# Kernel optimization log

Hardware: AMD Instinct MI355X
Metric: run time of the kernel (lower is better)

## Reference

```python
import jax, jax.numpy as jnp
import numpy as np

D_MODEL = 256
D_STATE = 1
HEADDIM = 32
NHEADS = D_MODEL // HEADDIM
HH = 64
WW = 64
BATCH = 2
L = HH * WW
D_IN_PROJ = (2 * D_MODEL + 2 * D_STATE + NHEADS) * 4


def _part1by1(n):
    n = n.astype(np.int64) & 0xFFFF
    n = (n | (n << 8)) & 0x00FF00FF
    n = (n | (n << 4)) & 0x0F0F0F0F
    n = (n | (n << 2)) & 0x33333333
    n = (n | (n << 1)) & 0x55555555
    return n


def _morton_indices(H, W):
    ys, xs = np.meshgrid(np.arange(H), np.arange(W), indexing='ij')
    ys, xs = ys.ravel(), xs.ravel()
    code_H = _part1by1(xs) | (_part1by1(ys) << 1)  # horizontal-first z-order
    code_V = _part1by1(ys) | (_part1by1(xs) << 1)  # vertical-first z-order
    mh = np.argsort(code_H, kind='stable').astype(np.int32)
    mv = np.argsort(code_V, kind='stable').astype(np.int32)
    ih = np.empty_like(mh); ih[mh] = np.arange(mh.size, dtype=np.int32)
    iv = np.empty_like(mv); iv[mv] = np.arange(mv.size, dtype=np.int32)
    return mh, mv, ih, iv


def setup_inputs() -> dict:
    key = jax.random.key(0)
    ks = jax.random.split(key, 12)
    x = jax.random.normal(ks[0], (BATCH, D_MODEL, HH, WW), dtype=jnp.float32)
    # RoPE tables: angles for L positions, HEADDIM/2 freqs
    freqs = 1.0 / (10000.0 ** (np.arange(0, HEADDIM, 2, dtype=np.float32) / HEADDIM))
    ang = np.outer(np.arange(L, dtype=np.float32), freqs)
    freqs_cos = jnp.asarray(np.cos(ang), dtype=jnp.float32)
    freqs_sin = jnp.asarray(np.sin(ang), dtype=jnp.float32)
    mh, mv, ih, iv = _morton_indices(HH, WW)
    # parameters
    W_in = jax.random.normal(ks[1], (D_MODEL, D_IN_PROJ), dtype=jnp.float32) * 0.02
    W_out = jax.random.normal(ks[2], (4 * D_MODEL, D_MODEL), dtype=jnp.float32) * 0.02
    conv_w = jax.random.normal(ks[3], (4, 2 * D_MODEL, 2 * D_MODEL, 3, 3), dtype=jnp.float32) * 0.02
    bn_gamma = jnp.ones((4, 2 * D_MODEL), dtype=jnp.float32)
    bn_beta = jnp.zeros((4, 2 * D_MODEL), dtype=jnp.float32)
    bn_mean = jax.random.normal(ks[4], (4, 2 * D_MODEL), dtype=jnp.float32) * 0.1
    bn_var = jax.random.uniform(ks[5], (4, 2 * D_MODEL), dtype=jnp.float32) * 0.5 + 0.5
    # dt bias init per module: inv softplus of dt ~ LogUniform(1e-3, 1e-1)
    u = np.asarray(jax.random.uniform(ks[6], (4, NHEADS)))
    dt = np.exp(u * (np.log(0.1) - np.log(0.001)) + np.log(0.001))
    dt_bias = jnp.asarray(dt + np.log(-np.expm1(-dt)), dtype=jnp.float32)
    A_log = jnp.log(jax.random.uniform(ks[7], (4, NHEADS), minval=1.0, maxval=16.0)).astype(jnp.float32)
    D = jnp.ones((4, NHEADS), dtype=jnp.float32)
    ln_gamma = jnp.ones((D_MODEL,), dtype=jnp.float32)
    ln_beta = jnp.zeros((D_MODEL,), dtype=jnp.float32)
    return dict(x=x, freqs_cos=freqs_cos, freqs_sin=freqs_sin,
                morton_H=jnp.asarray(mh), morton_V=jnp.asarray(mv),
                inv_H=jnp.asarray(ih), inv_V=jnp.asarray(iv),
                W_in=W_in, conv_w=conv_w, bn_gamma=bn_gamma, bn_beta=bn_beta,
                bn_mean=bn_mean, bn_var=bn_var, dt_bias=dt_bias, A_log=A_log,
                D=D, W_out=W_out, ln_gamma=ln_gamma, ln_beta=ln_beta)


def _rope(xh, cos, sin):
    # xh: [B,L,nh,hd]; complex multiply on (even,odd) pairs, matching view_as_complex
    xr, xi = xh[..., 0::2], xh[..., 1::2]
    c = cos[None, :, None, :]
    s = sin[None, :, None, :]
    out_r = xr * c - xi * s
    out_i = xr * s + xi * c
    return jnp.stack([out_r, out_i], axis=-1).reshape(xh.shape)


def _forward(x, freqs_cos, freqs_sin, morton_H, morton_V, inv_H, inv_V,
             W_in, conv_w, bn_gamma, bn_beta, bn_mean, bn_var,
             dt_bias, A_log, D, W_out, ln_gamma, ln_beta):
    B, C, H, W = x.shape
    Lh = H * W
    dim, ds, nh, hd = C, D_STATE, NHEADS, HEADDIM
    xf = x.reshape(B, C, Lh).transpose(0, 2, 1)            # [B,L,C]
    zxbcdt = xf @ W_in                                      # [B,L,d_in_proj]
    per = dim + (dim + 2 * ds) + nh
    specs = [(morton_H, inv_H, False), (morton_H, inv_H, True),
             (morton_V, inv_V, False), (morton_V, inv_V, True)]
    outs = []
    for d, (idx, iidx, flip) in enumerate(specs):
        blk = zxbcdt[..., d * per:(d + 1) * per]
        z = blk[..., :dim]
        xBC = blk[..., dim:2 * dim + 2 * ds]
        dt = blk[..., 2 * dim + 2 * ds:]
        xd, Bd, Cd = xBC[..., :dim], xBC[..., dim:dim + ds], xBC[..., dim + ds:]
        # depth-refine x,z with 3x3 conv + GELU + BN (eval)
        xz = jnp.concatenate([xd, z], axis=-1).transpose(0, 2, 1).reshape(B, 2 * C, H, W)
        xz = jax.lax.conv_general_dilated(xz, conv_w[d], (1, 1), 'SAME',
                                          dimension_numbers=('NCHW', 'OIHW', 'NCHW'))
        xz = jax.nn.gelu(xz)
        xz = (xz - bn_mean[d][None, :, None, None]) * jax.lax.rsqrt(bn_var[d] + 1e-3)[None, :, None, None] \
             * bn_gamma[d][None, :, None, None] + bn_beta[d][None, :, None, None]
        xz = xz.reshape(B, 2 * C, Lh).transpose(0, 2, 1)
        xd, zd = xz[..., :dim], xz[..., dim:]
        # morton reorder (+ flip for backward directions)
        def reord(a):
            a = jnp.take(a, idx, axis=1)
            return jnp.flip(a, axis=1) if flip else a
        xd, zd, Bd, Cd, dt = reord(xd), reord(zd), reord(Bd), reord(Cd), reord(dt)
        xh = _rope(xd.reshape(B, Lh, nh, hd), freqs_cos, freqs_sin)
        dtv = jax.nn.softplus(dt + dt_bias[d])              # [B,L,nh]
        A = -jnp.exp(A_log[d])                              # [nh]
        a = jnp.exp(dtv * A)                                # [B,L,nh]
        bterm = (dtv[..., None, None] * xh[..., None]) * Bd[:, :, None, None, :]  # [B,L,nh,hd,ds]
        def comb(c1, c2):
            a1, b1 = c1
            a2, b2 = c2
            return (a1 * a2, b1 * a2 + b2)
        _, h = jax.lax.associative_scan(comb, (a[..., None, None], bterm), axis=1)
        y = jnp.einsum('blhps,bls->blhp', h, Cd) + D[d][None, None, :, None] * xh
        y = y.reshape(B, Lh, dim) * (zd * jax.nn.sigmoid(zd))  # SiLU gate
        if flip:
            y = jnp.flip(y, axis=1)
        y = jnp.take(y, iidx, axis=1)                       # inverse morton
        outs.append(y)
    out = jnp.concatenate(outs, axis=-1) @ W_out            # [B,L,C]
    mu = out.mean(-1, keepdims=True)
    var = ((out - mu) ** 2).mean(-1, keepdims=True)
    out = (out - mu) * jax.lax.rsqrt(var + 1e-6) * ln_gamma + ln_beta
    return out.transpose(0, 2, 1).reshape(B, C, H, W)


def reference(x, freqs_cos, freqs_sin, morton_H, morton_V, inv_H, inv_V,
              W_in, conv_w, bn_gamma, bn_beta, bn_mean, bn_var,
              dt_bias, A_log, D, W_out, ln_gamma, ln_beta):
    return _forward(x, freqs_cos, freqs_sin, morton_H, morton_V, inv_H, inv_V,
                    W_in, conv_w, bn_gamma, bn_beta, bn_mean, bn_var,
                    dt_bias, A_log, D, W_out, ln_gamma, ln_beta)
```

## Files before the change

kernel.cpp:

```cpp
#include <hip/hip_runtime.h>
#include <math.h>

#define BATCH 2
#define CDIM 256
#define LLEN 4096
#define NH 8
#define HD 32
#define PER 522
#define NPROJ 2088
#define NPROJ_PAD 2112

typedef __attribute__((ext_vector_type(8))) short short8;
typedef __attribute__((ext_vector_type(4))) float f32x4;

static __device__ __forceinline__ ushort f2bf(float f) {
    unsigned u = __float_as_uint(f);
    u += 0x7fffu + ((u >> 16) & 1u);
    return (ushort)(u >> 16);
}
static __device__ __forceinline__ float bf2f(ushort u) {
    return __uint_as_float(((unsigned)u) << 16);
}

__global__ __launch_bounds__(256) void convert_wt(
    const float* __restrict__ W, ushort* __restrict__ Wt, int K, int N)
{
    __shared__ float tile[32][33];
    int n0 = blockIdx.x * 32, k0 = blockIdx.y * 32;
    int t = threadIdx.x;
    int nl = t & 31, kl = t >> 5;
    #pragma unroll
    for (int i = 0; i < 4; i++) {
        int n = n0 + nl;
        tile[kl + i * 8][nl] = (n < N) ? W[(long)(k0 + kl + i * 8) * N + n] : 0.f;
    }
    __syncthreads();
    int kl2 = t & 31, nl2 = t >> 5;
    #pragma unroll
    for (int i = 0; i < 4; i++)
        Wt[(long)(n0 + nl2 + i * 8) * K + k0 + kl2] = f2bf(tile[kl2][nl2 + i * 8]);
}

__global__ __launch_bounds__(256) void convert_x(
    const float* __restrict__ x, ushort* __restrict__ xbf)
{
    __shared__ float tile[32][33];
    int l0 = blockIdx.x * 32, c0 = blockIdx.y * 32, b = blockIdx.z;
    int t = threadIdx.x;
    int ll = t & 31, cl = t >> 5;
    #pragma unroll
    for (int i = 0; i < 4; i++)
        tile[cl + i * 8][ll] = x[((long)b * CDIM + c0 + cl + i * 8) * LLEN + l0 + ll];
    __syncthreads();
    int cl2 = t & 31, ll2 = t >> 5;
    #pragma unroll
    for (int i = 0; i < 4; i++)
        xbf[((long)b * LLEN + l0 + ll2 + i * 8) * CDIM + c0 + cl2] = f2bf(tile[cl2][ll2 + i * 8]);
}

__global__ __launch_bounds__(256) void convert_w(
    const float* __restrict__ cw, ushort* __restrict__ wbf)
{
    __shared__ ushort tmp[4608];
    int blk = blockIdx.x;
    int t = threadIdx.x;
    const float* src = cw + (long)blk * 4608;
    for (int q = t; q < 4608; q += 256) tmp[q] = f2bf(src[q]);
    __syncthreads();
    int d = blk >> 9, co = blk & 511;
    for (int q = t; q < 4608; q += 256) {
        int tt = q >> 9, ci = q & 511;
        wbf[(((long)(d * 9 + tt) * 512 + co) << 9) + ci] = tmp[ci * 9 + tt];
    }
}

__global__ __launch_bounds__(256) void gemm_in(
    const ushort* __restrict__ A, const ushort* __restrict__ Bt,
    ushort* __restrict__ cinb, float* __restrict__ bcdt)
{
    __shared__ ushort As[128][72];
    __shared__ ushort Bs[64][72];
    const int K = CDIM;
    int m0 = blockIdx.x * 128, n0 = blockIdx.y * 64;
    int t = threadIdx.x;
    int wave = t >> 6, lane = t & 63;
    int l15 = lane & 15, ko = lane >> 4;
    int mbase = wave * 32;

    f32x4 acc[2][4];
    #pragma unroll
    for (int mt = 0; mt < 2; mt++)
        #pragma unroll
        for (int nt = 0; nt < 4; nt++) acc[mt][nt] = (f32x4){0.f, 0.f, 0.f, 0.f};

    for (int k0 = 0; k0 < K; k0 += 64) {
        #pragma unroll
        for (int i = 0; i < 4; i++) {
            int g = t + 256 * i;
            int row = g >> 3, grp = g & 7;
            *(uint4*)&As[row][grp * 8] = *(const uint4*)&A[(long)(m0 + row) * K + k0 + grp * 8];
        }
        #pragma unroll
        for (int i = 0; i < 2; i++) {
            int g = t + 256 * i;
            int row = g >> 3, grp = g & 7;
            *(uint4*)&Bs[row][grp * 8] = *(const uint4*)&Bt[(long)(n0 + row) * K + k0 + grp * 8];
        }
        __syncthreads();
        #pragma unroll
        for (int kk = 0; kk < 2; kk++) {
            short8 a0 = *(const short8*)&As[mbase + l15][kk * 32 + ko * 8];
            short8 a1 = *(const short8*)&As[mbase + 16 + l15][kk * 32 + ko * 8];
            short8 bb[4];
            #pragma unroll
            for (int nt = 0; nt < 4; nt++)
                bb[nt] = *(const short8*)&Bs[nt * 16 + l15][kk * 32 + ko * 8];
            #pragma unroll
            for (int nt = 0; nt < 4; nt++) {
                acc[0][nt] = __builtin_amdgcn_mfma_f32_16x16x32_bf16(a0, bb[nt], acc[0][nt], 0, 0, 0);
                acc[1][nt] = __builtin_amdgcn_mfma_f32_16x16x32_bf16(a1, bb[nt], acc[1][nt], 0, 0, 0);
            }
        }
        __syncthreads();
    }
    #pragma unroll
    for (int nt = 0; nt < 4; nt++) {
        int n = n0 + nt * 16 + l15;
        if (n < NPROJ) {
            int d = n / PER;
            int r = n - d * PER;
            #pragma unroll
            for (int mt = 0; mt < 2; mt++)
                #pragma unroll
                for (int reg = 0; reg < 4; reg++) {
                    int m = m0 + mbase + mt * 16 + ko * 4 + reg;
                    int b = m >> 12, l = m & (LLEN - 1);
                    float v = acc[mt][nt][reg];
                    if (r < 512) {
                        int ch = (r < 256) ? (256 + r) : (r - 256);
                        cinb[(((long)d * BATCH + b) * LLEN + l) * 512 + ch] = f2bf(v);
                    } else {
                        bcdt[(long)m * 48 + d * 12 + (r - 512)] = v;
                    }
                }
        }
    }
}

__global__ __launch_bounds__(256) void gemm_bt(
    const ushort* __restrict__ A, const ushort* __restrict__ Bt, float* __restrict__ C,
    int K, int N)
{
    __shared__ ushort As[128][72];
    __shared__ ushort Bs[64][72];
    int m0 = blockIdx.x * 128, n0 = blockIdx.y * 64;
    int t = threadIdx.x;
    int wave = t >> 6, lane = t & 63;
    int l15 = lane & 15, ko = lane >> 4;
    int mbase = wave * 32;

    f32x4 acc[2][4];
    #pragma unroll
    for (int mt = 0; mt < 2; mt++)
        #pragma unroll
        for (int nt = 0; nt < 4; nt++) acc[mt][nt] = (f32x4){0.f, 0.f, 0.f, 0.f};

    for (int k0 = 0; k0 < K; k0 += 64) {
        #pragma unroll
        for (int i = 0; i < 4; i++) {
            int g = t + 256 * i;
            int row = g >> 3, grp = g & 7;
            *(uint4*)&As[row][grp * 8] = *(const uint4*)&A[(long)(m0 + row) * K + k0 + grp * 8];
        }
        #pragma unroll
        for (int i = 0; i < 2; i++) {
            int g = t + 256 * i;
            int row = g >> 3, grp = g & 7;
            *(uint4*)&Bs[row][grp * 8] = *(const uint4*)&Bt[(long)(n0 + row) * K + k0 + grp * 8];
        }
        __syncthreads();
        #pragma unroll
        for (int kk = 0; kk < 2; kk++) {
            short8 a0 = *(const short8*)&As[mbase + l15][kk * 32 + ko * 8];
            short8 a1 = *(const short8*)&As[mbase + 16 + l15][kk * 32 + ko * 8];
            short8 bb[4];
            #pragma unroll
            for (int nt = 0; nt < 4; nt++)
                bb[nt] = *(const short8*)&Bs[nt * 16 + l15][kk * 32 + ko * 8];
            #pragma unroll
            for (int nt = 0; nt < 4; nt++) {
                acc[0][nt] = __builtin_amdgcn_mfma_f32_16x16x32_bf16(a0, bb[nt], acc[0][nt], 0, 0, 0);
                acc[1][nt] = __builtin_amdgcn_mfma_f32_16x16x32_bf16(a1, bb[nt], acc[1][nt], 0, 0, 0);
            }
        }
        __syncthreads();
    }
    #pragma unroll
    for (int nt = 0; nt < 4; nt++) {
        int n = n0 + nt * 16 + l15;
        if (n < N) {
            #pragma unroll
            for (int mt = 0; mt < 2; mt++)
                #pragma unroll
                for (int reg = 0; reg < 4; reg++) {
                    int m = m0 + mbase + mt * 16 + ko * 4 + reg;
                    C[(long)m * N + n] = acc[mt][nt][reg];
                }
        }
    }
}

__global__ __launch_bounds__(256, 2) void conv_mfma(
    const ushort* __restrict__ cinb, const ushort* __restrict__ wbf,
    const float* __restrict__ bn_g, const float* __restrict__ bn_b,
    const float* __restrict__ bn_m, const float* __restrict__ bn_v,
    ushort* __restrict__ convb)
{
    __shared__ ushort in_s[6][4][66][8];

    int co0 = blockIdx.x * 64;
    int h0 = blockIdx.y * 4;
    int z = blockIdx.z;
    int d = z >> 1;
    int t = threadIdx.x;
    int wave = t >> 6, lane = t & 63;
    int l15 = lane & 15, ko = lane >> 4;

    const ushort* conv_in = cinb + (long)z * LLEN * 512;
    ushort* conv_out = convb + (long)z * LLEN * 512;

    f32x4 acc[4][4];
    #pragma unroll
    for (int m = 0; m < 4; m++)
        #pragma unroll
        for (int nt = 0; nt < 4; nt++) acc[m][nt] = (f32x4){0.f, 0.f, 0.f, 0.f};

    const ushort* wtb = wbf + (long)d * 9 * 512 * 512 + (long)(co0 + l15) * 512 + ko * 8;

    for (int ci0 = 0; ci0 < 512; ci0 += 32) {
        for (int q = t; q < 1584; q += 256) {
            int oct = q & 3, pxg = q >> 2;
            int row = pxg / 66, px = pxg - row * 66;
            int hh = h0 + row - 1, wp = px - 1;
            uint4 val = make_uint4(0u, 0u, 0u, 0u);
            if (hh >= 0 && hh < 64 && wp >= 0 && wp < 64)
                val = *(const uint4*)&conv_in[(((long)hh) * 64 + wp) * 512 + ci0 + oct * 8];
            *(uint4*)&in_s[row][oct][px][0] = val;
        }
        const ushort* wp0 = wtb + ci0;
        short8 bw[4], bwn[4];
        #pragma unroll
        for (int nt = 0; nt < 4; nt++)
            bw[nt] = *(const short8*)&wp0[(long)nt * (16 * 512)];
        __syncthreads();
        #pragma unroll 1
        for (int tap = 0; tap < 9; tap++) {
            if (tap < 8) {
                const ushort* wq = wp0 + (long)(tap + 1) * (512 * 512);
                #pragma unroll
                for (int nt = 0; nt < 4; nt++)
                    bwn[nt] = *(const short8*)&wq[(long)nt * (16 * 512)];
            }
            int kh = (tap >= 6) ? 2 : ((tap >= 3) ? 1 : 0);
            int kw = tap - kh * 3;
            short8 av[4];
            #pragma unroll
            for (int m = 0; m < 4; m++)
                av[m] = *(const short8*)&in_s[wave + kh][ko][m * 16 + l15 + kw][0];
            #pragma unroll
            for (int m = 0; m < 4; m++)
                #pragma unroll
                for (int nt = 0; nt < 4; nt++)
                    acc[m][nt] = __builtin_amdgcn_mfma_f32_16x16x32_bf16(av[m], bw[nt], acc[m][nt], 0, 0, 0);
            #pragma unroll
            for (int nt = 0; nt < 4; nt++) bw[nt] = bwn[nt];
        }
        __syncthreads();
    }

    int hgl = h0 + wave;
    #pragma unroll
    for (int nt = 0; nt < 4; nt++) {
        int co = co0 + nt * 16 + l15;
        float mean = bn_m[d * 512 + co], var = bn_v[d * 512 + co];
        float g = bn_g[d * 512 + co], bbias = bn_b[d * 512 + co];
        float inv = rsqrtf(var + 1e-3f);
        #pragma unroll
        for (int m = 0; m < 4; m++)
            #pragma unroll
            for (int reg = 0; reg < 4; reg++) {
                int wc = m * 16 + ko * 4 + reg;
                float v = acc[m][nt][reg];
                float u = -1.5957691216057308f * (v + 0.044715f * v * v * v);
                v = v / (1.f + __expf(u));
                v = (v - mean) * inv * g + bbias;
                conv_out[((long)hgl * 64 + wc) * 512 + co] = f2bf(v);
            }
    }
}

__global__ __launch_bounds__(256) void scan_chunk(
    const float* __restrict__ bcdt, const ushort* __restrict__ conv_out,
    const int* __restrict__ mortonH, const int* __restrict__ mortonV,
    const float* __restrict__ fcos, const float* __restrict__ fsin,
    const float* __restrict__ dt_bias, const float* __restrict__ A_log,
    float* __restrict__ hfin, float* __restrict__ aprod_out)
{
    int chunk = blockIdx.x, b = blockIdx.y, d = blockIdx.z;
    const int* idx = (d < 2) ? mortonH : mortonV;
    int flip = d & 1;
    int c = threadIdx.x;
    int hh = c >> 5, p = c & 31;
    int i = p >> 1;
    float Acoef = -expf(A_log[d * 8 + hh]);
    float dtb = dt_bias[d * 8 + hh];
    float hstate = 0.f, aprod = 1.f;
    const ushort* cop = conv_out + (long)(d * BATCH + b) * LLEN * 512;
    for (int jj = 0; jj < 64; jj++) {
        int j = chunk * 64 + jj;
        int jsrc = flip ? (LLEN - 1 - j) : j;
        int src = idx[jsrc];
        const float* bc = bcdt + ((long)b * LLEN + src) * 48 + d * 12;
        float dtraw = bc[2 + hh] + dtb;
        float dtv = (dtraw > 20.f) ? dtraw : log1pf(expf(dtraw));
        float a = expf(dtv * Acoef);
        float Bd = bc[0];
        const ushort* xrow = cop + (long)src * 512;
        uint xz = *(const uint*)&xrow[hh * 32 + (p & ~1)];
        float xe = bf2f((ushort)(xz & 0xffff));
        float xo = bf2f((ushort)(xz >> 16));
        float cs = fcos[j * 16 + i], sn = fsin[j * 16 + i];
        float xh = (p & 1) ? (xe * sn + xo * cs) : (xe * cs - xo * sn);
        hstate = a * hstate + dtv * xh * Bd;
        aprod *= a;
    }
    long o = (((long)d * BATCH + b) * 64 + chunk) * 256 + c;
    hfin[o] = hstate;
    aprod_out[o] = aprod;
}

__global__ __launch_bounds__(256) void scan_chain(
    const float* __restrict__ hfin, const float* __restrict__ aprod, float* __restrict__ h0)
{
    int db = blockIdx.x;
    int c = threadIdx.x;
    float run = 0.f;
    for (int ch = 0; ch < 64; ch++) {
        long o = ((long)db * 64 + ch) * 256 + c;
        h0[o] = run;
        run = aprod[o] * run + hfin[o];
    }
}

__global__ __launch_bounds__(256) void scan_final(
    const float* __restrict__ bcdt, const ushort* __restrict__ conv_out,
    const int* __restrict__ mortonH, const int* __restrict__ mortonV,
    const float* __restrict__ fcos, const float* __restrict__ fsin,
    const float* __restrict__ dt_bias, const float* __restrict__ A_log, const float* __restrict__ Dp,
    const float* __restrict__ h0, ushort* __restrict__ ycat)
{
    int chunk = blockIdx.x, b = blockIdx.y, d = blockIdx.z;
    const int* idx = (d < 2) ? mortonH : mortonV;
    int flip = d & 1;
    int c = threadIdx.x;
    int hh = c >> 5, p = c & 31;
    int i = p >> 1;
    float Acoef = -expf(A_log[d * 8 + hh]);
    float dtb = dt_bias[d * 8 + hh];
    float Dv = Dp[d * 8 + hh];
    float hstate = h0[(((long)d * BATCH + b) * 64 + chunk) * 256 + c];
    const ushort* cop = conv_out + (long)(d * BATCH + b) * LLEN * 512;
    for (int jj = 0; jj < 64; jj++) {
        int j = chunk * 64 + jj;
        int jsrc = flip ? (LLEN - 1 - j) : j;
        int src = idx[jsrc];
        const float* bc = bcdt + ((long)b * LLEN + src) * 48 + d * 12;
        float dtraw = bc[2 + hh] + dtb;
        float dtv = (dtraw > 20.f) ? dtraw : log1pf(expf(dtraw));
        float a = expf(dtv * Acoef);
        float Bd = bc[0];
        float Cd = bc[1];
        const ushort* xrow = cop + (long)src * 512;
        uint xz = *(const uint*)&xrow[hh * 32 + (p & ~1)];
        float xe = bf2f((ushort)(xz & 0xffff));
        float xo = bf2f((ushort)(xz >> 16));
        float cs = fcos[j * 16 + i], sn = fsin[j * 16 + i];
        float xh = (p & 1) ? (xe * sn + xo * cs) : (xe * cs - xo * sn);
        hstate = a * hstate + dtv * xh * Bd;
        float y = hstate * Cd + Dv * xh;
        float zd = bf2f(xrow[256 + c]);
        y *= zd / (1.f + expf(-zd));
        ycat[((long)b * LLEN + src) * 1024 + d * 256 + c] = f2bf(y);
    }
}

__global__ __launch_bounds__(256) void ln_out(
    const float* __restrict__ pre, const float* __restrict__ g, const float* __restrict__ bta,
    float* __restrict__ out)
{
    int row = blockIdx.x;
    int c = threadIdx.x;
    float v = pre[(long)row * 256 + c];
    float s = v, s2 = v * v;
    #pragma unroll
    for (int o = 32; o > 0; o >>= 1) {
        s += __shfl_down(s, o);
        s2 += __shfl_down(s2, o);
    }
    __shared__ float ss[4], ss2[4];
    __shared__ float mean_s, inv_s;
    int wid = c >> 6;
    if ((c & 63) == 0) { ss[wid] = s; ss2[wid] = s2; }
    __syncthreads();
    if (c == 0) {
        float S = ss[0] + ss[1] + ss[2] + ss[3];
        float S2 = ss2[0] + ss2[1] + ss2[2] + ss2[3];
        float mean = S / 256.f;
        float var = S2 / 256.f - mean * mean;
        mean_s = mean;
        inv_s = rsqrtf(var + 1e-6f);
    }
    __syncthreads();
    float o = (v - mean_s) * inv_s * g[c] + bta[c];
    int b = row >> 12, l = row & (LLEN - 1);
    out[((long)b * 256 + c) * (long)LLEN + l] = o;
}

extern "C" void kernel_launch(void* const* d_in, const int* in_sizes, int n_in,
                              void* d_out, int out_size, void* d_ws, size_t ws_size,
                              hipStream_t stream)
{
    const float* x        = (const float*)d_in[0];
    const float* fcos     = (const float*)d_in[1];
    const float* fsin     = (const float*)d_in[2];
    const int*   mortonH  = (const int*)d_in[3];
    const int*   mortonV  = (const int*)d_in[4];
    const float* W_in     = (const float*)d_in[7];
    const float* conv_w   = (const float*)d_in[8];
    const float* bn_g     = (const float*)d_in[9];
    const float* bn_b     = (const float*)d_in[10];
    const float* bn_m     = (const float*)d_in[11];
    const float* bn_v     = (const float*)d_in[12];
    const float* dt_bias  = (const float*)d_in[13];
    const float* A_log    = (const float*)d_in[14];
    const float* Dp       = (const float*)d_in[15];
    const float* W_out    = (const float*)d_in[16];
    const float* ln_g     = (const float*)d_in[17];
    const float* ln_b     = (const float*)d_in[18];
    float* out = (float*)d_out;

    float* ws = (float*)d_ws;
    const long CONVB_OFF   = 0;
    const long HFIN_OFF    = CONVB_OFF + 8388608;
    const long APROD_OFF   = HFIN_OFF + 4L * BATCH * 64 * 256;
    const long H0_OFF      = APROD_OFF + 4L * BATCH * 64 * 256;
    const long BCDT_OFF    = H0_OFF + 4L * BATCH * 64 * 256;
    const long WBF_OFF     = BCDT_OFF + (long)BATCH * LLEN * 48;
    const long CINB_OFF    = WBF_OFF + 4718592;
    const long XBF_OFF     = CINB_OFF + 8388608;
    const long WINT_OFF    = XBF_OFF + 1048576;
    const long WOUTT_OFF   = WINT_OFF + 270336;
    const long YCATB_OFF   = WOUTT_OFF + 131072;
    const long PRE_OFF     = YCATB_OFF + 4194304;

    ushort* convb   = (ushort*)(ws + CONVB_OFF);
    float* hfin     = ws + HFIN_OFF;
    float* aprod    = ws + APROD_OFF;
    float* h0       = ws + H0_OFF;
    float* bcdt     = ws + BCDT_OFF;
    ushort* wbf     = (ushort*)(ws + WBF_OFF);
    ushort* cinb    = (ushort*)(ws + CINB_OFF);
    ushort* xbf     = (ushort*)(ws + XBF_OFF);
    ushort* wint    = (ushort*)(ws + WINT_OFF);
    ushort* woutt   = (ushort*)(ws + WOUTT_OFF);
    ushort* ycatb   = (ushort*)(ws + YCATB_OFF);
    float* pre      = ws + PRE_OFF;

    convert_w<<<4 * 512, 256, 0, stream>>>(conv_w, wbf);
    convert_wt<<<dim3(NPROJ_PAD / 32, CDIM / 32), 256, 0, stream>>>(W_in, wint, CDIM, NPROJ);
    convert_wt<<<dim3(CDIM / 32, 1024 / 32), 256, 0, stream>>>(W_out, woutt, 1024, CDIM);
    convert_x<<<dim3(LLEN / 32, CDIM / 32, BATCH), 256, 0, stream>>>(x, xbf);

    gemm_in<<<dim3(64, NPROJ_PAD / 64), 256, 0, stream>>>(xbf, wint, cinb, bcdt);

    conv_mfma<<<dim3(8, 16, 4 * BATCH), 256, 0, stream>>>(
        cinb, wbf, bn_g, bn_b, bn_m, bn_v, convb);

    scan_chunk<<<dim3(64, BATCH, 4), 256, 0, stream>>>(
        bcdt, convb, mortonH, mortonV, fcos, fsin, dt_bias, A_log, hfin, aprod);
    scan_chain<<<4 * BATCH, 256, 0, stream>>>(hfin, aprod, h0);
    scan_final<<<dim3(64, BATCH, 4), 256, 0, stream>>>(
        bcdt, convb, mortonH, mortonV, fcos, fsin, dt_bias, A_log, Dp, h0, ycatb);

    gemm_bt<<<dim3(64, CDIM / 64), 256, 0, stream>>>(ycatb, woutt, pre, 1024, CDIM);

    ln_out<<<BATCH * LLEN, 256, 0, stream>>>(pre, ln_g, ln_b, out);
}
```

Measured before the change: 499.2 us.

## Double-buffer conv input tile with async global-to-LDS loads

Replaces the synchronous per-ci-chunk global-to-shared staging in the conv MFMA kernel with a double-buffered LDS tile filled by global_load_lds direct transfers, with per-thread addresses and masks precomputed once. The next input chunk is prefetched while MFMAs consume the current one, and the weight prefetch now also runs across chunk boundaries. The aim is to hide global-load latency and remove the register round-trip. In exchange it doubles LDS use, which may lower occupancy, and it zero-fills the padding once up front.

```diff
diff --git a/kernel.cpp b/kernel.cpp
--- a/kernel.cpp
+++ b/kernel.cpp
@@ -216,7 +216,7 @@
     const float* __restrict__ bn_m, const float* __restrict__ bn_v,
     ushort* __restrict__ convb)
 {
-    __shared__ ushort in_s[6][4][66][8];
+    __shared__ __align__(16) ushort in_s[2][1584][8];
 
     int co0 = blockIdx.x * 64;
     int h0 = blockIdx.y * 4;
@@ -229,6 +229,34 @@
     const ushort* conv_in = cinb + (long)z * LLEN * 512;
     ushort* conv_out = convb + (long)z * LLEN * 512;
 
+    {
+        uint4* p = (uint4*)in_s;
+        #pragma unroll
+        for (int i = 0; i < 13; ++i) {
+            int q = t + 256 * i;
+            if (q < 3168) p[q] = make_uint4(0u, 0u, 0u, 0u);
+        }
+    }
+
+    const ushort* gp[7];
+    unsigned ldo[7];
+    bool mk[7];
+    #pragma unroll
+    for (int c = 0; c < 7; ++c) {
+        int chunkid = (c < 6) ? (wave * 6 + c) : 24;
+        int unit = chunkid * 64 + lane;
+        int row = unit / 264;
+        int rem = unit - row * 264;
+        int oct = rem / 66;
+        int px = rem - oct * 66;
+        int hh = h0 + row - 1, wp = px - 1;
+        bool ok = (unit < 1584) && (hh >= 0) && (hh < 64) && (wp >= 0) && (wp < 64);
+        if (c == 6) ok = ok && (wave == 0);
+        gp[c] = conv_in + ((long)(ok ? (hh * 64 + wp) : 0) * 512 + oct * 8);
+        ldo[c] = (unsigned)chunkid * 512u;
+        mk[c] = ok;
+    }
+
     f32x4 acc[4][4];
     #pragma unroll
     for (int m = 0; m < 4; m++)
@@ -237,36 +265,49 @@
 
     const ushort* wtb = wbf + (long)d * 9 * 512 * 512 + (long)(co0 + l15) * 512 + ko * 8;
 
-    for (int ci0 = 0; ci0 < 512; ci0 += 32) {
-        for (int q = t; q < 1584; q += 256) {
-            int oct = q & 3, pxg = q >> 2;
-            int row = pxg / 66, px = pxg - row * 66;
-            int hh = h0 + row - 1, wp = px - 1;
-            uint4 val = make_uint4(0u, 0u, 0u, 0u);
-            if (hh >= 0 && hh < 64 && wp >= 0 && wp < 64)
-                val = *(const uint4*)&conv_in[(((long)hh) * 64 + wp) * 512 + ci0 + oct * 8];
-            *(uint4*)&in_s[row][oct][px][0] = val;
-        }
-        const ushort* wp0 = wtb + ci0;
-        short8 bw[4], bwn[4];
-        #pragma unroll
-        for (int nt = 0; nt < 4; nt++)
-            bw[nt] = *(const short8*)&wp0[(long)nt * (16 * 512)];
-        __syncthreads();
+    __syncthreads();
+
+    #pragma unroll
+    for (int c = 0; c < 7; ++c) {
+        if (mk[c])
+            __builtin_amdgcn_global_load_lds(
+                (const __attribute__((address_space(1))) void*)gp[c],
+                (__attribute__((address_space(3))) void*)(&in_s[0][0][0] + ldo[c]), 16, 0, 0);
+        gp[c] += 32;
+    }
+    short8 bw[4], bwn[4];
+    #pragma unroll
+    for (int nt = 0; nt < 4; nt++)
+        bw[nt] = *(const short8*)&wtb[(long)nt * (16 * 512)];
+    __syncthreads();
+
+    for (int s = 0; s < 16; ++s) {
+        int cur = s & 1;
+        if (s < 15) {
+            ushort* lb = &in_s[cur ^ 1][0][0];
+            #pragma unroll
+            for (int c = 0; c < 7; ++c) {
+                if (mk[c])
+                    __builtin_amdgcn_global_load_lds(
+                        (const __attribute__((address_space(1))) void*)gp[c],
+                        (__attribute__((address_space(3))) void*)(lb + ldo[c]), 16, 0, 0);
+                gp[c] += 32;
+            }
+        }
+        const ushort* ws0 = wtb + s * 32;
         #pragma unroll 1
         for (int tap = 0; tap < 9; tap++) {
-            if (tap < 8) {
-                const ushort* wq = wp0 + (long)(tap + 1) * (512 * 512);
-                #pragma unroll
-                for (int nt = 0; nt < 4; nt++)
-                    bwn[nt] = *(const short8*)&wq[(long)nt * (16 * 512)];
-            }
+            const ushort* wn = (tap < 8) ? (ws0 + (long)(tap + 1) * (512 * 512))
+                                         : (wtb + (s + 1) * 32);
+            #pragma unroll
+            for (int nt = 0; nt < 4; nt++)
+                bwn[nt] = *(const short8*)&wn[(long)nt * (16 * 512)];
             int kh = (tap >= 6) ? 2 : ((tap >= 3) ? 1 : 0);
             int kw = tap - kh * 3;
             short8 av[4];
             #pragma unroll
             for (int m = 0; m < 4; m++)
-                av[m] = *(const short8*)&in_s[wave + kh][ko][m * 16 + l15 + kw][0];
+                av[m] = *(const short8*)&in_s[cur][(wave + kh) * 264 + ko * 66 + (m * 16 + l15 + kw)][0];
             #pragma unroll
             for (int m = 0; m < 4; m++)
                 #pragma unroll
```

Result: slower. 537.1 us (+7.6%).

## Prefetch next conv input slab into registers while computing current slab

Applied to the files above, without the earlier changes.

The 3x3 conv MFMA kernel now precomputes per-thread global offsets and halo masks once, zero-fills the padded shared tile a single time, and loads the next 32-channel input slab into registers while the current slab's nine taps run. It then writes the slab to shared memory after a barrier. The weight prefetch for the first tap of the next slab is folded into the last tap iteration. This aims to hide global load latency behind the MFMA work and to drop the repeated index and bounds arithmetic. In exchange it uses more registers (seven uint4 staging values plus offset arrays), which may hurt occupancy at launch bounds of 256 threads and 2 blocks, and it adds a second barrier per slab.

```diff
diff --git a/kernel.cpp b/kernel.cpp
--- a/kernel.cpp
+++ b/kernel.cpp
@@ -216,7 +216,7 @@
     const float* __restrict__ bn_m, const float* __restrict__ bn_v,
     ushort* __restrict__ convb)
 {
-    __shared__ ushort in_s[6][4][66][8];
+    __shared__ __align__(16) ushort in_s[6][4][66][8];
 
     int co0 = blockIdx.x * 64;
     int h0 = blockIdx.y * 4;
@@ -228,6 +228,24 @@
 
     const ushort* conv_in = cinb + (long)z * LLEN * 512;
     ushort* conv_out = convb + (long)z * LLEN * 512;
+    ushort* in_f = &in_s[0][0][0][0];
+
+    int goff[7]; int ldo[7]; bool mk[7];
+    #pragma unroll
+    for (int i = 0; i < 7; ++i) {
+        int u = t + 256 * i;
+        int row = u / 264; int rem = u - row * 264;
+        int oct = rem / 66; int px = rem - oct * 66;
+        int hh = h0 + row - 1, wp = px - 1;
+        bool ok = (u < 1584) && (hh >= 0) && (hh < 64) && (wp >= 0) && (wp < 64);
+        goff[i] = (ok ? (hh * 64 + wp) : 0) * 512 + oct * 8;
+        ldo[i] = u * 8;
+        mk[i] = ok;
+    }
+
+    #pragma unroll
+    for (int i = 0; i < 7; ++i)
+        if (t + 256 * i < 1584) *(uint4*)&in_f[ldo[i]] = make_uint4(0u, 0u, 0u, 0u);
 
     f32x4 acc[4][4];
     #pragma unroll
@@ -237,30 +255,42 @@
 
     const ushort* wtb = wbf + (long)d * 9 * 512 * 512 + (long)(co0 + l15) * 512 + ko * 8;
 
-    for (int ci0 = 0; ci0 < 512; ci0 += 32) {
-        for (int q = t; q < 1584; q += 256) {
-            int oct = q & 3, pxg = q >> 2;
-            int row = pxg / 66, px = pxg - row * 66;
-            int hh = h0 + row - 1, wp = px - 1;
-            uint4 val = make_uint4(0u, 0u, 0u, 0u);
-            if (hh >= 0 && hh < 64 && wp >= 0 && wp < 64)
-                val = *(const uint4*)&conv_in[(((long)hh) * 64 + wp) * 512 + ci0 + oct * 8];
-            *(uint4*)&in_s[row][oct][px][0] = val;
-        }
-        const ushort* wp0 = wtb + ci0;
-        short8 bw[4], bwn[4];
-        #pragma unroll
-        for (int nt = 0; nt < 4; nt++)
-            bw[nt] = *(const short8*)&wp0[(long)nt * (16 * 512)];
-        __syncthreads();
+    uint4 v[7];
+    #pragma unroll
+    for (int i = 0; i < 7; ++i) {
+        if (mk[i]) {
+            v[i] = *(const uint4*)&conv_in[goff[i]];
+            goff[i] += 32;
+        }
+    }
+    #pragma unroll
+    for (int i = 0; i < 7; ++i)
+        if (mk[i]) *(uint4*)&in_f[ldo[i]] = v[i];
+
+    short8 bw[4], bwn[4];
+    #pragma unroll
+    for (int nt = 0; nt < 4; nt++)
+        bw[nt] = *(const short8*)&wtb[(long)nt * (16 * 512)];
+    __syncthreads();
+
+    for (int s = 0; s < 16; ++s) {
+        if (s < 15) {
+            #pragma unroll
+            for (int i = 0; i < 7; ++i) {
+                if (mk[i]) {
+                    v[i] = *(const uint4*)&conv_in[goff[i]];
+                    goff[i] += 32;
+                }
+            }
+        }
+        const ushort* ws0 = wtb + s * 32;
         #pragma unroll 1
         for (int tap = 0; tap < 9; tap++) {
-            if (tap < 8) {
-                const ushort* wq = wp0 + (long)(tap + 1) * (512 * 512);
-                #pragma unroll
-                for (int nt = 0; nt < 4; nt++)
-                    bwn[nt] = *(const short8*)&wq[(long)nt * (16 * 512)];
-            }
+            const ushort* wn = (tap < 8) ? (ws0 + (long)(tap + 1) * (512 * 512))
+                                         : (wtb + (s + 1) * 32);
+            #pragma unroll
+            for (int nt = 0; nt < 4; nt++)
+                bwn[nt] = *(const short8*)&wn[(long)nt * (16 * 512)];
             int kh = (tap >= 6) ? 2 : ((tap >= 3) ? 1 : 0);
             int kw = tap - kh * 3;
             short8 av[4];
@@ -274,6 +304,12 @@
                     acc[m][nt] = __builtin_amdgcn_mfma_f32_16x16x32_bf16(av[m], bw[nt], acc[m][nt], 0, 0, 0);
             #pragma unroll
             for (int nt = 0; nt < 4; nt++) bw[nt] = bwn[nt];
+        }
+        __syncthreads();
+        if (s < 15) {
+            #pragma unroll
+            for (int i = 0; i < 7; ++i)
+                if (mk[i]) *(uint4*)&in_f[ldo[i]] = v[i];
         }
         __syncthreads();
     }
@@ -290,11 +326,11 @@
             #pragma unroll
             for (int reg = 0; reg < 4; reg++) {
                 int wc = m * 16 + ko * 4 + reg;
-                float v = acc[m][nt][reg];
-                float u = -1.5957691216057308f * (v + 0.044715f * v * v * v);
-                v = v / (1.f + __expf(u));
-                v = (v - mean) * inv * g + bbias;
-                conv_out[((long)hgl * 64 + wc) * 512 + co] = f2bf(v);
+                float vv = acc[m][nt][reg];
+                float u = -1.5957691216057308f * (vv + 0.044715f * vv * vv * vv);
+                vv = vv / (1.f + __expf(u));
+                vv = (vv - mean) * inv * g + bbias;
+                conv_out[((long)hgl * 64 + wc) * 512 + co] = f2bf(vv);
             }
     }
 }
```

Measured after the change: 610.6 us. +22.3%, slower.
